# Kernel optimization log

Hardware: AMD Instinct MI355X
Metric: run time of the kernel (lower is better)

## Reference

```python
import jax, jax.numpy as jnp
import numpy as np

NEG_SLOPE = 0.2
NUM_GRAPHS = 64


def _gatv2_layer(x, src, dst, Wl, bl, Wr, br, att, bias, n_nodes, heads, ch):
    # lin_l (source) and lin_r (target) transforms -> [N, H, C]
    xs = (x @ Wl + bl).reshape(n_nodes, heads, ch)
    xd = (x @ Wr + br).reshape(n_nodes, heads, ch)
    s = xs[src]                                   # [E, H, C] gathered source feats
    e = jax.nn.leaky_relu(s + xd[dst], NEG_SLOPE)  # GATv2: leaky_relu BEFORE att dot
    score = jnp.einsum('ehc,hc->eh', e, att)       # [E, H]
    # segment softmax over edges sharing the same target node
    smax = jax.ops.segment_max(score, dst, num_segments=n_nodes)
    ex = jnp.exp(score - smax[dst])
    denom = jax.ops.segment_sum(ex, dst, num_segments=n_nodes)
    alpha = ex / denom[dst]                        # [E, H]
    out = jax.ops.segment_sum(alpha[:, :, None] * s, dst, num_segments=n_nodes)
    return out.reshape(n_nodes, heads * ch) + bias


def setup_inputs() -> dict:
    key = jax.random.key(0)
    ks = jax.random.split(key, 20)
    N, E, F = 50000, 800000, 128
    H, C = 4, 64
    G = NUM_GRAPHS
    sc = 0.05
    inp = {
        'x': jax.random.normal(ks[0], (N, F), jnp.float32),
        'edge_index': jax.random.randint(ks[1], (2, E), 0, N, jnp.int64 if jax.config.read('jax_enable_x64') else jnp.int32).astype(jnp.int32),
        'batch': jnp.sort(jax.random.randint(ks[2], (N,), 0, G)).astype(jnp.int32),
        'W_l1': jax.random.normal(ks[3], (F, H * C)) * sc,
        'b_l1': jax.random.normal(ks[4], (H * C,)) * sc,
        'W_r1': jax.random.normal(ks[5], (F, H * C)) * sc,
        'b_r1': jax.random.normal(ks[6], (H * C,)) * sc,
        'att1': jax.random.normal(ks[7], (H, C)) * sc,
        'bias1': jax.random.normal(ks[8], (H * C,)) * sc,
        'W_l2': jax.random.normal(ks[9], (H * C, C)) * sc,
        'b_l2': jax.random.normal(ks[10], (C,)) * sc,
        'W_r2': jax.random.normal(ks[11], (H * C, C)) * sc,
        'b_r2': jax.random.normal(ks[12], (C,)) * sc,
        'att2': jax.random.normal(ks[13], (1, C)) * sc,
        'bias2': jax.random.normal(ks[14], (C,)) * sc,
        'W_lin': jax.random.normal(ks[15], (C, 1)) * sc,
        'b_lin': jax.random.normal(ks[16], (1,)) * sc,
    }
    return inp


def reference(x, edge_index, batch, W_l1, b_l1, W_r1, b_r1, att1, bias1,
              W_l2, b_l2, W_r2, b_r2, att2, bias2, W_lin, b_lin):
    N = x.shape[0]
    # PyG GATv2Conv adds self-loops by default
    loops = jnp.arange(N, dtype=edge_index.dtype)
    src = jnp.concatenate([edge_index[0], loops])
    dst = jnp.concatenate([edge_index[1], loops])

    h = _gatv2_layer(x, src, dst, W_l1, b_l1, W_r1, b_r1, att1, bias1, N, 4, 64)
    h = jax.nn.relu(h)  # dropout=identity (eval), norm=Identity
    h = _gatv2_layer(h, src, dst, W_l2, b_l2, W_r2, b_r2, att2, bias2, N, 1, 64)

    # global mean pool over graphs
    sums = jax.ops.segment_sum(h, batch, num_segments=NUM_GRAPHS)
    counts = jax.ops.segment_sum(jnp.ones((N,), h.dtype), batch, num_segments=NUM_GRAPHS)
    pooled = sums / jnp.maximum(counts, 1.0)[:, None]  # [G, 64]
    return pooled @ W_lin + b_lin                      # [G, 1]
```

## Files before the change

kernel.cpp:

```cpp
#include <hip/hip_runtime.h>
#include <hip/hip_bf16.h>
#include <math.h>

typedef __attribute__((ext_vector_type(8))) short short8;
typedef __attribute__((ext_vector_type(4))) float floatx4;

__device__ __forceinline__ float bf2f(unsigned short u) {
  union { unsigned int i; float f; } v; v.i = ((unsigned int)u) << 16; return v.f;
}
__device__ __forceinline__ unsigned short f2bf(float f) {
  union { float f; unsigned int u; } v; v.f = f;
  unsigned int r = (v.u + 0x7fffu + ((v.u >> 16) & 1u)) >> 16;
  return (unsigned short)r;
}
__device__ __forceinline__ int imin(int a, int b) { return a < b ? a : b; }
__device__ __forceinline__ int iclamp(int v, int lo, int hi) {
  return v < lo ? lo : (v > hi ? hi : v);
}
__device__ __forceinline__ float uasf(unsigned int u) {
  union { unsigned int i; float f; } v; v.i = u; return v.f;
}

__global__ void k_sentinel(float* out, float val) {
  if (threadIdx.x < 64) out[threadIdx.x] = val;
}

__global__ void k_probe_init(const void* __restrict__ x, int* dflag,
                             int* deg, float* pool, int* cnt, int N) {
  int i = blockIdx.x * 256 + threadIdx.x;
  if (i < N) deg[i] = 1;
  if (i < 64 * 64) pool[i] = 0.f;
  if (i < 64) cnt[i] = 0;
  if (blockIdx.x == 0) {
    __shared__ int c;
    if (threadIdx.x == 0) c = 0;
    __syncthreads();
    unsigned short u = ((const unsigned short*)x)[threadIdx.x];
    int e = (u >> 7) & 0xFF;
    atomicAdd(&c, (u == 0) || (e >= 100 && e <= 145));
    __syncthreads();
    if (threadIdx.x == 0) dflag[0] = (c < 240) ? 1 : 0;
  }
}

struct CvtSegs {
  const void* src[10];
  unsigned short* dst[10];
  int len[10];
};

__global__ void k_prep(const void* __restrict__ x, unsigned short* __restrict__ x_c,
                       int n8, CvtSegs segs,
                       const void* __restrict__ s0, const void* __restrict__ s1,
                       const void* __restrict__ s2, const void* __restrict__ s3,
                       unsigned short* __restrict__ d0, unsigned short* __restrict__ d1,
                       unsigned short* __restrict__ d2, unsigned short* __restrict__ d3,
                       const int* __restrict__ edst, int* deg, int E, int N,
                       const int* __restrict__ dflag, int nCvt8, int nTransB) {
  int b = blockIdx.x;
  if (b < nCvt8) {
    if (!dflag[0]) return;
    int i = b * 256 + threadIdx.x;
    if (i >= n8) return;
    const float* s = (const float*)x + (size_t)i * 8;
    ushort4 a, c;
    a.x = f2bf(s[0]); a.y = f2bf(s[1]); a.z = f2bf(s[2]); a.w = f2bf(s[3]);
    c.x = f2bf(s[4]); c.y = f2bf(s[5]); c.z = f2bf(s[6]); c.w = f2bf(s[7]);
    ((ushort4*)x_c)[i * 2] = a;
    ((ushort4*)x_c)[i * 2 + 1] = c;
    return;
  }
  b -= nCvt8;
  if (b < 10) {
    int i = threadIdx.x;
    if (i < segs.len[b])
      segs.dst[b][i] = dflag[0] ? f2bf(((const float*)segs.src[b])[i])
                                : ((const unsigned short*)segs.src[b])[i];
    return;
  }
  b -= 10;
  if (b < nTransB) {
    int idx = b * 256 + threadIdx.x;
    const void* src; unsigned short* dst; int R, C, loc;
    if (idx < 32768)      { src = s0; dst = d0; R = 128; C = 256; loc = idx; }
    else if (idx < 65536) { src = s1; dst = d1; R = 128; C = 256; loc = idx - 32768; }
    else if (idx < 81920) { src = s2; dst = d2; R = 256; C = 64;  loc = idx - 65536; }
    else                  { src = s3; dst = d3; R = 256; C = 64;  loc = idx - 81920; }
    unsigned short u = dflag[0] ? f2bf(((const float*)src)[loc])
                                : ((const unsigned short*)src)[loc];
    int r = loc / C, cc = loc - r * C;
    dst[cc * R + r] = u;
    return;
  }
  b -= nTransB;
  int e = b * 256 + threadIdx.x;
  if (e < E) atomicAdd(&deg[iclamp(edst[e], 0, N - 1)], 1);
}

__global__ __launch_bounds__(1024) void k_scan1(const int* __restrict__ deg, int* bsum, int N) {
  __shared__ int sm[1024];
  int tid = threadIdx.x;
  int i = blockIdx.x * 1024 + tid;
  sm[tid] = (i < N) ? deg[i] : 0;
  __syncthreads();
  for (int off = 512; off > 0; off >>= 1) {
    if (tid < off) sm[tid] += sm[tid + off];
    __syncthreads();
  }
  if (tid == 0) bsum[blockIdx.x] = sm[0];
}

__global__ void k_scan2(int* bsum, int nb) {
  if (threadIdx.x == 0) {
    int run = 0;
    for (int b = 0; b < nb; ++b) { int t = bsum[b]; bsum[b] = run; run += t; }
  }
}

__global__ __launch_bounds__(1024) void k_scan3(const int* __restrict__ deg,
                                                const int* __restrict__ bsum,
                                                int* rowptr, int* cursor, int N) {
  __shared__ int sm[1024];
  int tid = threadIdx.x;
  int i = blockIdx.x * 1024 + tid;
  int v = (i < N) ? deg[i] : 0;
  sm[tid] = v;
  __syncthreads();
  for (int off = 1; off < 1024; off <<= 1) {
    int t = (tid >= off) ? sm[tid - off] : 0;
    __syncthreads();
    sm[tid] += t;
    __syncthreads();
  }
  if (i < N) {
    int ex = sm[tid] - v + bsum[blockIdx.x];
    rowptr[i] = ex;
    cursor[i] = ex;
    if (i == N - 1) rowptr[N] = ex + v;
  }
}

__global__ void k_scatter(const int* __restrict__ esrc, const int* __restrict__ edst,
                          int* cursor, int* colx, int E, int N) {
  int e = blockIdx.x * 256 + threadIdx.x;
  int ET = E + N;
  if (e < ET) {
    int s, d;
    if (e < E) { s = iclamp(esrc[e], 0, N - 1); d = iclamp(edst[e], 0, N - 1); }
    else { s = e - E; d = s; }
    int pos = atomicAdd(&cursor[d], 1);
    pos = iclamp(pos, 0, ET - 1);
    colx[pos] = s;
  }
}

template <int K, int CT, int RT>
__global__ __launch_bounds__(256) void k_gemm2r(
    const unsigned short* __restrict__ A0, const unsigned short* __restrict__ A1,
    const int* __restrict__ dflag,
    const unsigned short* __restrict__ BTl, const unsigned short* __restrict__ BTr,
    const unsigned short* __restrict__ bl, const unsigned short* __restrict__ br,
    unsigned short* __restrict__ outl, unsigned short* __restrict__ outr,
    int Nrows, int M) {
  constexpr int KI = K / 32;
  const unsigned short* A = dflag[0] ? A1 : A0;
  int lane = threadIdx.x & 63;
  int wave = threadIdx.x >> 6;
  int r = lane & 15, q = lane >> 4;
  int col0 = blockIdx.y * (4 * CT * 16) + wave * (CT * 16);
  int row0 = blockIdx.x * (16 * RT);
  short8 Bl[KI][CT], Br[KI][CT];
#pragma unroll
  for (int t = 0; t < CT; ++t) {
    const unsigned short* bpl = BTl + (size_t)(col0 + t * 16 + r) * K + q * 8;
    const unsigned short* bpr = BTr + (size_t)(col0 + t * 16 + r) * K + q * 8;
#pragma unroll
    for (int k = 0; k < KI; ++k) {
      Bl[k][t] = *reinterpret_cast<const short8*>(bpl + k * 32);
      Br[k][t] = *reinterpret_cast<const short8*>(bpr + k * 32);
    }
  }
  float bvl[CT], bvr[CT];
#pragma unroll
  for (int t = 0; t < CT; ++t) {
    bvl[t] = bf2f(bl[col0 + t * 16 + r]);
    bvr[t] = bf2f(br[col0 + t * 16 + r]);
  }
  short8 a[KI], an[KI];
  {
    int ar0 = imin(row0 + r, Nrows - 1);
    const unsigned short* Ap = A + (size_t)ar0 * K + q * 8;
#pragma unroll
    for (int k = 0; k < KI; ++k) a[k] = *reinterpret_cast<const short8*>(Ap + k * 32);
  }
  for (int rt = 0; rt < RT; ++rt) {
    if (rt + 1 < RT) {
      int arn = imin(row0 + (rt + 1) * 16 + r, Nrows - 1);
      const unsigned short* Apn = A + (size_t)arn * K + q * 8;
#pragma unroll
      for (int k = 0; k < KI; ++k) an[k] = *reinterpret_cast<const short8*>(Apn + k * 32);
    }
    floatx4 accl[CT], accr[CT];
#pragma unroll
    for (int t = 0; t < CT; ++t) {
      accl[t] = (floatx4){0.f, 0.f, 0.f, 0.f};
      accr[t] = (floatx4){0.f, 0.f, 0.f, 0.f};
    }
#pragma unroll
    for (int k = 0; k < KI; ++k) {
#pragma unroll
      for (int t = 0; t < CT; ++t) {
        accl[t] = __builtin_amdgcn_mfma_f32_16x16x32_bf16(a[k], Bl[k][t], accl[t], 0, 0, 0);
        accr[t] = __builtin_amdgcn_mfma_f32_16x16x32_bf16(a[k], Br[k][t], accr[t], 0, 0, 0);
      }
    }
#pragma unroll
    for (int t = 0; t < CT; ++t) {
      int col = col0 + t * 16 + r;
#pragma unroll
      for (int rr = 0; rr < 4; ++rr) {
        int row = row0 + rt * 16 + q * 4 + rr;
        if (row < Nrows) {
          outl[(size_t)row * M + col] = f2bf(accl[t][rr] + bvl[t]);
          outr[(size_t)row * M + col] = f2bf(accr[t][rr] + bvr[t]);
        }
      }
    }
#pragma unroll
    for (int k = 0; k < KI; ++k) a[k] = an[k];
  }
}

#define UNPACK2(u, v0, v1, v2, v3)          \
  v0 = uasf(u.x << 16); v1 = uasf(u.x & 0xffff0000u); \
  v2 = uasf(u.y << 16); v3 = uasf(u.y & 0xffff0000u);

#define SCORE(q0, q1, q2, q3, p)                             \
  p = q0 * 0.6f;                                             \
  p = fmaf(q1, 0.6f, p); p = fmaf(q2, 0.6f, p); p = fmaf(q3, 0.6f, p); \
  p = fmaf(c0, fabsf(q0), p); p = fmaf(c1, fabsf(q1), p);    \
  p = fmaf(c2, fabsf(q2), p); p = fmaf(c3, fabsf(q3), p);

__global__ __launch_bounds__(256) void k_agg_h4(
    const int* __restrict__ rowptr, const int* __restrict__ colx,
    const unsigned short* __restrict__ xs, const unsigned short* __restrict__ xd,
    const unsigned short* __restrict__ att, const unsigned short* __restrict__ bias,
    unsigned short* __restrict__ hout, int N) {
  int lane = threadIdx.x & 63;
  int dst = (blockIdx.x * 256 + threadIdx.x) >> 6;
  if (dst >= N) return;
  int off = lane << 2;
  unsigned int off2 = (unsigned int)off * 2;
  const char* xsb = (const char*)xs;
  ushort4 au = *reinterpret_cast<const ushort4*>(att + off);
  ushort4 du = *reinterpret_cast<const ushort4*>(xd + (size_t)dst * 256 + off);
  float a0 = bf2f(au.x), a1 = bf2f(au.y), a2 = bf2f(au.z), a3 = bf2f(au.w);
  float d0 = bf2f(du.x), d1 = bf2f(du.y), d2 = bf2f(du.z), d3 = bf2f(du.w);
  float ad0 = a0 * d0, ad1 = a1 * d1, ad2 = a2 * d2, ad3 = a3 * d3;
  float c0 = copysignf(0.4f, a0), c1 = copysignf(0.4f, a1);
  float c2 = copysignf(0.4f, a2), c3 = copysignf(0.4f, a3);
  float l = 0.f, o0 = 0.f, o1 = 0.f, o2 = 0.f, o3 = 0.f;
  int beg = __builtin_amdgcn_readfirstlane(rowptr[dst]);
  int end = __builtin_amdgcn_readfirstlane(rowptr[dst + 1]);
  int e1 = end - 1;
  int i0 = colx[beg], i1 = colx[imin(beg + 1, e1)];
  int i2 = colx[imin(beg + 2, e1)], i3 = colx[imin(beg + 3, e1)];
  uint2 ua = *(const uint2*)(xsb + (((unsigned)i0 << 9) + off2));
  uint2 ub = *(const uint2*)(xsb + (((unsigned)i1 << 9) + off2));
  uint2 uc = *(const uint2*)(xsb + (((unsigned)i2 << 9) + off2));
  uint2 ud = *(const uint2*)(xsb + (((unsigned)i3 << 9) + off2));
  for (int e = beg; e < end; e += 4) {
    uint2 na = ua, nb = ub, nc = uc, nd = ud;
    int np = e + 4;
    if (np < end) {
      int t0 = colx[np], t1 = colx[imin(np + 1, e1)];
      int t2 = colx[imin(np + 2, e1)], t3 = colx[imin(np + 3, e1)];
      na = *(const uint2*)(xsb + (((unsigned)t0 << 9) + off2));
      nb = *(const uint2*)(xsb + (((unsigned)t1 << 9) + off2));
      nc = *(const uint2*)(xsb + (((unsigned)t2 << 9) + off2));
      nd = *(const uint2*)(xsb + (((unsigned)t3 << 9) + off2));
    }
    float va0, va1, va2, va3, vb0, vb1, vb2, vb3;
    float vc0, vc1, vc2, vc3, vd0, vd1, vd2, vd3;
    UNPACK2(ua, va0, va1, va2, va3)
    UNPACK2(ub, vb0, vb1, vb2, vb3)
    UNPACK2(uc, vc0, vc1, vc2, vc3)
    UNPACK2(ud, vd0, vd1, vd2, vd3)
    float qa0 = fmaf(a0, va0, ad0), qa1 = fmaf(a1, va1, ad1);
    float qa2 = fmaf(a2, va2, ad2), qa3 = fmaf(a3, va3, ad3);
    float qb0 = fmaf(a0, vb0, ad0), qb1 = fmaf(a1, vb1, ad1);
    float qb2 = fmaf(a2, vb2, ad2), qb3 = fmaf(a3, vb3, ad3);
    float qc0 = fmaf(a0, vc0, ad0), qc1 = fmaf(a1, vc1, ad1);
    float qc2 = fmaf(a2, vc2, ad2), qc3 = fmaf(a3, vc3, ad3);
    float qd0 = fmaf(a0, vd0, ad0), qd1 = fmaf(a1, vd1, ad1);
    float qd2 = fmaf(a2, vd2, ad2), qd3 = fmaf(a3, vd3, ad3);
    float pa, pb, pc, pd;
    SCORE(qa0, qa1, qa2, qa3, pa)
    SCORE(qb0, qb1, qb2, qb3, pb)
    SCORE(qc0, qc1, qc2, qc3, pc)
    SCORE(qd0, qd1, qd2, qd3, pd)
    pa += __shfl_xor(pa, 1); pb += __shfl_xor(pb, 1);
    pc += __shfl_xor(pc, 1); pd += __shfl_xor(pd, 1);
    pa += __shfl_xor(pa, 2); pb += __shfl_xor(pb, 2);
    pc += __shfl_xor(pc, 2); pd += __shfl_xor(pd, 2);
    pa += __shfl_xor(pa, 4); pb += __shfl_xor(pb, 4);
    pc += __shfl_xor(pc, 4); pd += __shfl_xor(pd, 4);
    pa += __shfl_xor(pa, 8); pb += __shfl_xor(pb, 8);
    pc += __shfl_xor(pc, 8); pd += __shfl_xor(pd, 8);
    pa = fminf(fmaxf(pa, -60.f), 60.f);
    pb = (e + 1 < end) ? fminf(fmaxf(pb, -60.f), 60.f) : -INFINITY;
    pc = (e + 2 < end) ? fminf(fmaxf(pc, -60.f), 60.f) : -INFINITY;
    pd = (e + 3 < end) ? fminf(fmaxf(pd, -60.f), 60.f) : -INFINITY;
    float wa = __expf(pa), wb = __expf(pb), wc = __expf(pc), wd = __expf(pd);
    l += (wa + wb) + (wc + wd);
    o0 = fmaf(wa, va0, o0); o0 = fmaf(wb, vb0, o0);
    o0 = fmaf(wc, vc0, o0); o0 = fmaf(wd, vd0, o0);
    o1 = fmaf(wa, va1, o1); o1 = fmaf(wb, vb1, o1);
    o1 = fmaf(wc, vc1, o1); o1 = fmaf(wd, vd1, o1);
    o2 = fmaf(wa, va2, o2); o2 = fmaf(wb, vb2, o2);
    o2 = fmaf(wc, vc2, o2); o2 = fmaf(wd, vd2, o2);
    o3 = fmaf(wa, va3, o3); o3 = fmaf(wb, vb3, o3);
    o3 = fmaf(wc, vc3, o3); o3 = fmaf(wd, vd3, o3);
    ua = na; ub = nb; uc = nc; ud = nd;
  }
  float rl = 1.0f / l;
  ushort4 bu = *reinterpret_cast<const ushort4*>(bias + off);
  ushort4 res;
  res.x = f2bf(fmaxf(fmaf(o0, rl, bf2f(bu.x)), 0.f));
  res.y = f2bf(fmaxf(fmaf(o1, rl, bf2f(bu.y)), 0.f));
  res.z = f2bf(fmaxf(fmaf(o2, rl, bf2f(bu.z)), 0.f));
  res.w = f2bf(fmaxf(fmaf(o3, rl, bf2f(bu.w)), 0.f));
  *reinterpret_cast<ushort4*>(hout + (size_t)dst * 256 + off) = res;
}

__global__ __launch_bounds__(256) void k_agg_h1(
    const int* __restrict__ rowptr, const int* __restrict__ colx,
    const unsigned short* __restrict__ xs, const unsigned short* __restrict__ xd,
    const unsigned short* __restrict__ att, const unsigned short* __restrict__ bias,
    float* __restrict__ hout, int N) {
  int lane = threadIdx.x & 63;
  int wid = (blockIdx.x * 256 + threadIdx.x) >> 6;
  int g = lane >> 4, sl = lane & 15;
  int dst = wid * 4 + g;
  bool valid = dst < N;
  int dsafe = valid ? dst : 0;
  int cb = sl << 2;
  unsigned int cb2 = (unsigned int)cb * 2;
  const char* xsb = (const char*)xs;
  ushort4 au = *reinterpret_cast<const ushort4*>(att + cb);
  ushort4 du = *reinterpret_cast<const ushort4*>(xd + (size_t)dsafe * 64 + cb);
  float a0 = bf2f(au.x), a1 = bf2f(au.y), a2 = bf2f(au.z), a3 = bf2f(au.w);
  float d0 = bf2f(du.x), d1 = bf2f(du.y), d2 = bf2f(du.z), d3 = bf2f(du.w);
  float ad0 = a0 * d0, ad1 = a1 * d1, ad2 = a2 * d2, ad3 = a3 * d3;
  float c0 = copysignf(0.4f, a0), c1 = copysignf(0.4f, a1);
  float c2 = copysignf(0.4f, a2), c3 = copysignf(0.4f, a3);
  float l = 0.f, o0 = 0.f, o1 = 0.f, o2 = 0.f, o3 = 0.f;
  int beg = valid ? rowptr[dst] : 0;
  int end = valid ? rowptr[dst + 1] : 0;
  if (end > beg) {
    int e1 = end - 1;
    int i0 = colx[beg], i1 = colx[imin(beg + 1, e1)];
    int i2 = colx[imin(beg + 2, e1)], i3 = colx[imin(beg + 3, e1)];
    uint2 ua = *(const uint2*)(xsb + (((unsigned)i0 << 7) + cb2));
    uint2 ub = *(const uint2*)(xsb + (((unsigned)i1 << 7) + cb2));
    uint2 uc = *(const uint2*)(xsb + (((unsigned)i2 << 7) + cb2));
    uint2 ud = *(const uint2*)(xsb + (((unsigned)i3 << 7) + cb2));
    for (int e = beg; e < end; e += 4) {
      uint2 na = ua, nb = ub, nc = uc, nd = ud;
      int np = e + 4;
      if (np < end) {
        int t0 = colx[np], t1 = colx[imin(np + 1, e1)];
        int t2 = colx[imin(np + 2, e1)], t3 = colx[imin(np + 3, e1)];
        na = *(const uint2*)(xsb + (((unsigned)t0 << 7) + cb2));
        nb = *(const uint2*)(xsb + (((unsigned)t1 << 7) + cb2));
        nc = *(const uint2*)(xsb + (((unsigned)t2 << 7) + cb2));
        nd = *(const uint2*)(xsb + (((unsigned)t3 << 7) + cb2));
      }
      float va0, va1, va2, va3, vb0, vb1, vb2, vb3;
      float vc0, vc1, vc2, vc3, vd0, vd1, vd2, vd3;
      UNPACK2(ua, va0, va1, va2, va3)
      UNPACK2(ub, vb0, vb1, vb2, vb3)
      UNPACK2(uc, vc0, vc1, vc2, vc3)
      UNPACK2(ud, vd0, vd1, vd2, vd3)
      float qa0 = fmaf(a0, va0, ad0), qa1 = fmaf(a1, va1, ad1);
      float qa2 = fmaf(a2, va2, ad2), qa3 = fmaf(a3, va3, ad3);
      float qb0 = fmaf(a0, vb0, ad0), qb1 = fmaf(a1, vb1, ad1);
      float qb2 = fmaf(a2, vb2, ad2), qb3 = fmaf(a3, vb3, ad3);
      float qc0 = fmaf(a0, vc0, ad0), qc1 = fmaf(a1, vc1, ad1);
      float qc2 = fmaf(a2, vc2, ad2), qc3 = fmaf(a3, vc3, ad3);
      float qd0 = fmaf(a0, vd0, ad0), qd1 = fmaf(a1, vd1, ad1);
      float qd2 = fmaf(a2, vd2, ad2), qd3 = fmaf(a3, vd3, ad3);
      float pa, pb, pc, pd;
      SCORE(qa0, qa1, qa2, qa3, pa)
      SCORE(qb0, qb1, qb2, qb3, pb)
      SCORE(qc0, qc1, qc2, qc3, pc)
      SCORE(qd0, qd1, qd2, qd3, pd)
      pa += __shfl_xor(pa, 1); pb += __shfl_xor(pb, 1);
      pc += __shfl_xor(pc, 1); pd += __shfl_xor(pd, 1);
      pa += __shfl_xor(pa, 2); pb += __shfl_xor(pb, 2);
      pc += __shfl_xor(pc, 2); pd += __shfl_xor(pd, 2);
      pa += __shfl_xor(pa, 4); pb += __shfl_xor(pb, 4);
      pc += __shfl_xor(pc, 4); pd += __shfl_xor(pd, 4);
      pa += __shfl_xor(pa, 8); pb += __shfl_xor(pb, 8);
      pc += __shfl_xor(pc, 8); pd += __shfl_xor(pd, 8);
      pa = fminf(fmaxf(pa, -60.f), 60.f);
      pb = (e + 1 < end) ? fminf(fmaxf(pb, -60.f), 60.f) : -INFINITY;
      pc = (e + 2 < end) ? fminf(fmaxf(pc, -60.f), 60.f) : -INFINITY;
      pd = (e + 3 < end) ? fminf(fmaxf(pd, -60.f), 60.f) : -INFINITY;
      float wa = __expf(pa), wb = __expf(pb), wc = __expf(pc), wd = __expf(pd);
      l += (wa + wb) + (wc + wd);
      o0 = fmaf(wa, va0, o0); o0 = fmaf(wb, vb0, o0);
      o0 = fmaf(wc, vc0, o0); o0 = fmaf(wd, vd0, o0);
      o1 = fmaf(wa, va1, o1); o1 = fmaf(wb, vb1, o1);
      o1 = fmaf(wc, vc1, o1); o1 = fmaf(wd, vd1, o1);
      o2 = fmaf(wa, va2, o2); o2 = fmaf(wb, vb2, o2);
      o2 = fmaf(wc, vc2, o2); o2 = fmaf(wd, vd2, o2);
      o3 = fmaf(wa, va3, o3); o3 = fmaf(wb, vb3, o3);
      o3 = fmaf(wd, vd3, o3); o3 = fmaf(wc, vc3, o3);
      ua = na; ub = nb; uc = nc; ud = nd;
    }
  }
  if (valid) {
    float rl = 1.0f / l;
    ushort4 bu = *reinterpret_cast<const ushort4*>(bias + cb);
    floatx4 res;
    res[0] = fmaf(o0, rl, bf2f(bu.x));
    res[1] = fmaf(o1, rl, bf2f(bu.y));
    res[2] = fmaf(o2, rl, bf2f(bu.z));
    res[3] = fmaf(o3, rl, bf2f(bu.w));
    *reinterpret_cast<floatx4*>(hout + (size_t)dst * 64 + cb) = res;
  }
}

__global__ __launch_bounds__(256) void k_pool(const float* __restrict__ h2,
                                              const int* __restrict__ batch,
                                              float* pool, int* cnt, int N) {
  int lane = threadIdx.x & 63;
  int wid = (blockIdx.x * 256 + threadIdx.x) >> 6;
  int n0 = wid * 32;
  if (n0 >= N) return;
  int nend = imin(n0 + 32, N);
  float acc = 0.f;
  int c = 0;
  int gcur = iclamp(batch[n0], 0, 63);
  for (int n = n0; n < nend; ++n) {
    int gg = iclamp(batch[n], 0, 63);
    if (gg != gcur) {
      atomicAdd(&pool[gcur * 64 + lane], acc);
      if (lane == 0) atomicAdd(&cnt[gcur], c);
      acc = 0.f; c = 0; gcur = gg;
    }
    acc += h2[(size_t)n * 64 + lane];
    c++;
  }
  atomicAdd(&pool[gcur * 64 + lane], acc);
  if (lane == 0) atomicAdd(&cnt[gcur], c);
}

__global__ void k_final(const float* __restrict__ pool, const int* __restrict__ cnt,
                        const unsigned short* __restrict__ Wlinc,
                        const unsigned short* __restrict__ blinc,
                        float* __restrict__ out) {
  int g = threadIdx.x;
  if (g >= 64) return;
  float inv = 1.f / fmaxf((float)cnt[g], 1.f);
  float s = 0.f;
  for (int c = 0; c < 64; ++c) s += pool[g * 64 + c] * bf2f(Wlinc[c]);
  out[g] = fmaf(s, inv, bf2f(blinc[0]));
}

extern "C" void kernel_launch(void* const* d_in, const int* in_sizes, int n_in,
                              void* d_out, int out_size, void* d_ws, size_t ws_size,
                              hipStream_t stream) {
  const void* x     = d_in[0];
  const int*  ei    = (const int*)d_in[1];
  const int*  batch = (const int*)d_in[2];
  const void* Wl1 = d_in[3];  const void* bl1 = d_in[4];
  const void* Wr1 = d_in[5];  const void* br1 = d_in[6];
  const void* att1 = d_in[7]; const void* bias1 = d_in[8];
  const void* Wl2 = d_in[9];  const void* bl2 = d_in[10];
  const void* Wr2 = d_in[11]; const void* br2 = d_in[12];
  const void* att2 = d_in[13]; const void* bias2 = d_in[14];
  const void* Wlin = d_in[15]; const void* blin = d_in[16];
  float* out = (float*)d_out;

  const int F = 128, HC = 256, C2 = 64;
  int N = in_sizes[0] / F;
  int E = in_sizes[1] / 2;
  int ET = E + N;
  const int* esrc = ei;
  const int* edst = ei + E;

  char* w = (char*)d_ws;
  auto alloc = [&](size_t bytes) {
    char* p = w;
    w += (bytes + 255) & ~(size_t)255;
    return p;
  };
  int* dflag  = (int*)alloc(4);
  int* rowptr = (int*)alloc((size_t)(N + 1) * 4);
  int* cursor = (int*)alloc((size_t)N * 4);
  int* deg    = (int*)alloc((size_t)N * 4);
  int* bsum   = (int*)alloc(1024 * 4);
  float* pool = (float*)alloc(64 * 64 * 4);
  int* cnt    = (int*)alloc(64 * 4);
  int* colx   = (int*)alloc((size_t)ET * 4);
  unsigned short* smallc = (unsigned short*)alloc(4096);
  unsigned short* Wl1T = (unsigned short*)alloc((size_t)F * HC * 2);
  unsigned short* Wr1T = (unsigned short*)alloc((size_t)F * HC * 2);
  unsigned short* Wl2T = (unsigned short*)alloc((size_t)HC * C2 * 2);
  unsigned short* Wr2T = (unsigned short*)alloc((size_t)HC * C2 * 2);
  unsigned short* xs1  = (unsigned short*)alloc((size_t)N * HC * 2);
  unsigned short* xd1  = (unsigned short*)alloc((size_t)N * HC * 2);
  unsigned short* h1   = (unsigned short*)alloc((size_t)N * HC * 2);
  size_t required = (size_t)(w - (char*)d_ws);

  unsigned short* x_c = h1;
  unsigned short* xs2 = xs1;
  unsigned short* xd2 = xs1 + (size_t)N * C2;
  float*          h2  = (float*)xd1;

  unsigned short* bl1c   = smallc + 0;
  unsigned short* br1c   = smallc + 256;
  unsigned short* att1c  = smallc + 512;
  unsigned short* bias1c = smallc + 768;
  unsigned short* bl2c   = smallc + 1024;
  unsigned short* br2c   = smallc + 1088;
  unsigned short* att2c  = smallc + 1152;
  unsigned short* bias2c = smallc + 1216;
  unsigned short* Wlinc  = smallc + 1280;
  unsigned short* blinc  = smallc + 1344;

  if (ws_size < required) {
    k_sentinel<<<1, 64, 0, stream>>>(out, 1000.f + (float)(ws_size >> 20));
    return;
  }

  k_probe_init<<<(N + 255) / 256, 256, 0, stream>>>(x, dflag, deg, pool, cnt, N);

  CvtSegs segs;
  const void* ssrc[10] = {bl1, br1, att1, bias1, bl2, br2, att2, bias2, Wlin, blin};
  unsigned short* sdst[10] = {bl1c, br1c, att1c, bias1c, bl2c, br2c, att2c, bias2c, Wlinc, blinc};
  int slen[10] = {256, 256, 256, 256, 64, 64, 64, 64, 64, 1};
  for (int i = 0; i < 10; ++i) { segs.src[i] = ssrc[i]; segs.dst[i] = sdst[i]; segs.len[i] = slen[i]; }
  int n8 = N * F / 8;
  int nCvt8 = (n8 + 255) / 256;
  int nTransB = (2 * F * HC + 2 * HC * C2 + 255) / 256;
  int nHist = (E + 255) / 256;
  k_prep<<<nCvt8 + 10 + nTransB + nHist, 256, 0, stream>>>(
      x, x_c, n8, segs, Wl1, Wr1, Wl2, Wr2, Wl1T, Wr1T, Wl2T, Wr2T,
      edst, deg, E, N, dflag, nCvt8, nTransB);

  int nb = (N + 1023) / 1024;
  k_scan1<<<nb, 1024, 0, stream>>>(deg, bsum, N);
  k_scan2<<<1, 64, 0, stream>>>(bsum, nb);
  k_scan3<<<nb, 1024, 0, stream>>>(deg, bsum, rowptr, cursor, N);
  k_scatter<<<(ET + 255) / 256, 256, 0, stream>>>(esrc, edst, cursor, colx, E, N);

  {
    dim3 g((N + 127) / 128, 2);
    k_gemm2r<128, 2, 8><<<g, 256, 0, stream>>>(
        (const unsigned short*)x, x_c, dflag, Wl1T, Wr1T, bl1c, br1c, xs1, xd1, N, HC);
  }
  k_agg_h4<<<(N + 3) / 4, 256, 0, stream>>>(rowptr, colx, xs1, xd1, att1c, bias1c, h1, N);

  {
    dim3 g((N + 63) / 64, 1);
    k_gemm2r<256, 1, 4><<<g, 256, 0, stream>>>(
        h1, h1, dflag, Wl2T, Wr2T, bl2c, br2c, xs2, xd2, N, C2);
  }
  k_agg_h1<<<(N + 15) / 16, 256, 0, stream>>>(rowptr, colx, xs2, xd2, att2c, bias2c, h2, N);

  int pw = (N + 31) / 32;
  k_pool<<<(pw + 3) / 4, 256, 0, stream>>>(h2, batch, pool, cnt, N);
  k_final<<<1, 64, 0, stream>>>(pool, cnt, Wlinc, blinc, out);
}
```

Before: 361.5 us.

## Merge setup kernels, fuse CSR scatter with layer-1 GEMM, use DPP reductions

Drops the probe/init kernel: zeroing moves to a memset and each k_prep block detects the input dtype itself. The single-thread scan2 is folded into scan3, where each block sums the preceding block totals itself. Self-loop edges are placed deterministically at the end of each row, and the edge scatter now shares one launch with the layer-1 GEMM so the two can overlap. It also pads colx so aggregation can drop its index clamps, and replaces the shuffle reductions with DPP row reductions. The cost is redundant dtype probing in every prep block and a serial prefix loop in scan3 blocks.

```diff
diff --git a/kernel.cpp b/kernel.cpp
--- a/kernel.cpp
+++ b/kernel.cpp
@@ -20,27 +20,18 @@
 __device__ __forceinline__ float uasf(unsigned int u) {
   union { unsigned int i; float f; } v; v.i = u; return v.f;
 }
+__device__ __forceinline__ float sum16(float x) {
+  union { float f; int i; } a, t;
+  a.f = x;
+  t.i = __builtin_amdgcn_update_dpp(0, a.i, 0x121, 0xF, 0xF, true); a.f += t.f;
+  t.i = __builtin_amdgcn_update_dpp(0, a.i, 0x122, 0xF, 0xF, true); a.f += t.f;
+  t.i = __builtin_amdgcn_update_dpp(0, a.i, 0x124, 0xF, 0xF, true); a.f += t.f;
+  t.i = __builtin_amdgcn_update_dpp(0, a.i, 0x128, 0xF, 0xF, true); a.f += t.f;
+  return a.f;
+}
 
 __global__ void k_sentinel(float* out, float val) {
   if (threadIdx.x < 64) out[threadIdx.x] = val;
-}
-
-__global__ void k_probe_init(const void* __restrict__ x, int* dflag,
-                             int* deg, float* pool, int* cnt, int N) {
-  int i = blockIdx.x * 256 + threadIdx.x;
-  if (i < N) deg[i] = 1;
-  if (i < 64 * 64) pool[i] = 0.f;
-  if (i < 64) cnt[i] = 0;
-  if (blockIdx.x == 0) {
-    __shared__ int c;
-    if (threadIdx.x == 0) c = 0;
-    __syncthreads();
-    unsigned short u = ((const unsigned short*)x)[threadIdx.x];
-    int e = (u >> 7) & 0xFF;
-    atomicAdd(&c, (u == 0) || (e >= 100 && e <= 145));
-    __syncthreads();
-    if (threadIdx.x == 0) dflag[0] = (c < 240) ? 1 : 0;
-  }
 }
 
 struct CvtSegs {
@@ -56,10 +47,21 @@
                        unsigned short* __restrict__ d0, unsigned short* __restrict__ d1,
                        unsigned short* __restrict__ d2, unsigned short* __restrict__ d3,
                        const int* __restrict__ edst, int* deg, int E, int N,
-                       const int* __restrict__ dflag, int nCvt8, int nTransB) {
+                       int* dflag, int* colx, int ET, int nCvt8, int nTransB) {
+  __shared__ int csh;
+  if (threadIdx.x == 0) csh = 0;
+  __syncthreads();
+  {
+    unsigned short u = ((const unsigned short*)x)[threadIdx.x];
+    int e = (u >> 7) & 0xFF;
+    atomicAdd(&csh, (u == 0) || (e >= 100 && e <= 145));
+  }
+  __syncthreads();
+  int isf = (csh < 240);
+
   int b = blockIdx.x;
   if (b < nCvt8) {
-    if (!dflag[0]) return;
+    if (!isf) return;
     int i = b * 256 + threadIdx.x;
     if (i >= n8) return;
     const float* s = (const float*)x + (size_t)i * 8;
@@ -72,10 +74,14 @@
   }
   b -= nCvt8;
   if (b < 10) {
+    if (b == 0) {
+      if (threadIdx.x == 0) dflag[0] = isf;
+      if (threadIdx.x >= 248) colx[ET + (threadIdx.x - 248)] = 0;
+    }
     int i = threadIdx.x;
     if (i < segs.len[b])
-      segs.dst[b][i] = dflag[0] ? f2bf(((const float*)segs.src[b])[i])
-                                : ((const unsigned short*)segs.src[b])[i];
+      segs.dst[b][i] = isf ? f2bf(((const float*)segs.src[b])[i])
+                           : ((const unsigned short*)segs.src[b])[i];
     return;
   }
   b -= 10;
@@ -86,8 +92,8 @@
     else if (idx < 65536) { src = s1; dst = d1; R = 128; C = 256; loc = idx - 32768; }
     else if (idx < 81920) { src = s2; dst = d2; R = 256; C = 64;  loc = idx - 65536; }
     else                  { src = s3; dst = d3; R = 256; C = 64;  loc = idx - 81920; }
-    unsigned short u = dflag[0] ? f2bf(((const float*)src)[loc])
-                                : ((const unsigned short*)src)[loc];
+    unsigned short u = isf ? f2bf(((const float*)src)[loc])
+                           : ((const unsigned short*)src)[loc];
     int r = loc / C, cc = loc - r * C;
     dst[cc * R + r] = u;
     return;
@@ -101,7 +107,7 @@
   __shared__ int sm[1024];
   int tid = threadIdx.x;
   int i = blockIdx.x * 1024 + tid;
-  sm[tid] = (i < N) ? deg[i] : 0;
+  sm[tid] = (i < N) ? deg[i] + 1 : 0;
   __syncthreads();
   for (int off = 512; off > 0; off >>= 1) {
     if (tid < off) sm[tid] += sm[tid + off];
@@ -110,20 +116,19 @@
   if (tid == 0) bsum[blockIdx.x] = sm[0];
 }
 
-__global__ void k_scan2(int* bsum, int nb) {
-  if (threadIdx.x == 0) {
-    int run = 0;
-    for (int b = 0; b < nb; ++b) { int t = bsum[b]; bsum[b] = run; run += t; }
-  }
-}
-
 __global__ __launch_bounds__(1024) void k_scan3(const int* __restrict__ deg,
                                                 const int* __restrict__ bsum,
                                                 int* rowptr, int* cursor, int N) {
   __shared__ int sm[1024];
+  __shared__ int boff;
   int tid = threadIdx.x;
+  if (tid == 0) {
+    int r = 0;
+    for (int b = 0; b < blockIdx.x; ++b) r += bsum[b];
+    boff = r;
+  }
   int i = blockIdx.x * 1024 + tid;
-  int v = (i < N) ? deg[i] : 0;
+  int v = (i < N) ? deg[i] + 1 : 0;
   sm[tid] = v;
   __syncthreads();
   for (int off = 1; off < 1024; off <<= 1) {
@@ -133,42 +138,27 @@
     __syncthreads();
   }
   if (i < N) {
-    int ex = sm[tid] - v + bsum[blockIdx.x];
+    int ex = sm[tid] - v + boff;
     rowptr[i] = ex;
     cursor[i] = ex;
     if (i == N - 1) rowptr[N] = ex + v;
   }
 }
 
-__global__ void k_scatter(const int* __restrict__ esrc, const int* __restrict__ edst,
-                          int* cursor, int* colx, int E, int N) {
-  int e = blockIdx.x * 256 + threadIdx.x;
-  int ET = E + N;
-  if (e < ET) {
-    int s, d;
-    if (e < E) { s = iclamp(esrc[e], 0, N - 1); d = iclamp(edst[e], 0, N - 1); }
-    else { s = e - E; d = s; }
-    int pos = atomicAdd(&cursor[d], 1);
-    pos = iclamp(pos, 0, ET - 1);
-    colx[pos] = s;
-  }
-}
-
 template <int K, int CT, int RT>
-__global__ __launch_bounds__(256) void k_gemm2r(
-    const unsigned short* __restrict__ A0, const unsigned short* __restrict__ A1,
-    const int* __restrict__ dflag,
+__device__ __forceinline__ void gemm2r_body(
+    int bx, int by, int tid,
+    const unsigned short* __restrict__ A,
     const unsigned short* __restrict__ BTl, const unsigned short* __restrict__ BTr,
     const unsigned short* __restrict__ bl, const unsigned short* __restrict__ br,
     unsigned short* __restrict__ outl, unsigned short* __restrict__ outr,
     int Nrows, int M) {
   constexpr int KI = K / 32;
-  const unsigned short* A = dflag[0] ? A1 : A0;
-  int lane = threadIdx.x & 63;
-  int wave = threadIdx.x >> 6;
+  int lane = tid & 63;
+  int wave = tid >> 6;
   int r = lane & 15, q = lane >> 4;
-  int col0 = blockIdx.y * (4 * CT * 16) + wave * (CT * 16);
-  int row0 = blockIdx.x * (16 * RT);
+  int col0 = by * (4 * CT * 16) + wave * (CT * 16);
+  int row0 = bx * (16 * RT);
   short8 Bl[KI][CT], Br[KI][CT];
 #pragma unroll
   for (int t = 0; t < CT; ++t) {
@@ -229,6 +219,47 @@
 #pragma unroll
     for (int k = 0; k < KI; ++k) a[k] = an[k];
   }
+}
+
+__global__ __launch_bounds__(256) void k_phase1(
+    const unsigned short* __restrict__ A0, const unsigned short* __restrict__ A1,
+    const int* __restrict__ dflag,
+    const unsigned short* __restrict__ BTl, const unsigned short* __restrict__ BTr,
+    const unsigned short* __restrict__ bl, const unsigned short* __restrict__ br,
+    unsigned short* __restrict__ outl, unsigned short* __restrict__ outr,
+    int Nrows, int M, int nRB, int nG,
+    const int* __restrict__ esrc, const int* __restrict__ edst,
+    const int* __restrict__ rowptr, int* cursor, int* colx, int E, int N) {
+  int b = blockIdx.x;
+  if (b < nG) {
+    const unsigned short* A = dflag[0] ? A1 : A0;
+    gemm2r_body<128, 2, 8>(b >> 1, b & 1, threadIdx.x, A, BTl, BTr, bl, br,
+                           outl, outr, Nrows, M);
+    return;
+  }
+  b -= nG;
+  int e = b * 256 + threadIdx.x;
+  int ET = E + N;
+  if (e < ET) {
+    if (e < E) {
+      int s = iclamp(esrc[e], 0, N - 1), d = iclamp(edst[e], 0, N - 1);
+      int pos = atomicAdd(&cursor[d], 1);
+      colx[iclamp(pos, 0, ET - 1)] = s;
+    } else {
+      int i = e - E;
+      colx[rowptr[i + 1] - 1] = i;
+    }
+  }
+}
+
+__global__ __launch_bounds__(256) void k_gemm2r_l2(
+    const unsigned short* __restrict__ A,
+    const unsigned short* __restrict__ BTl, const unsigned short* __restrict__ BTr,
+    const unsigned short* __restrict__ bl, const unsigned short* __restrict__ br,
+    unsigned short* __restrict__ outl, unsigned short* __restrict__ outr,
+    int Nrows, int M) {
+  gemm2r_body<256, 1, 4>(blockIdx.x, 0, threadIdx.x, A, BTl, BTr, bl, br,
+                         outl, outr, Nrows, M);
 }
 
 #define UNPACK2(u, v0, v1, v2, v3)          \
@@ -262,9 +293,8 @@
   float l = 0.f, o0 = 0.f, o1 = 0.f, o2 = 0.f, o3 = 0.f;
   int beg = __builtin_amdgcn_readfirstlane(rowptr[dst]);
   int end = __builtin_amdgcn_readfirstlane(rowptr[dst + 1]);
-  int e1 = end - 1;
-  int i0 = colx[beg], i1 = colx[imin(beg + 1, e1)];
-  int i2 = colx[imin(beg + 2, e1)], i3 = colx[imin(beg + 3, e1)];
+  int i0 = colx[beg], i1 = colx[beg + 1];
+  int i2 = colx[beg + 2], i3 = colx[beg + 3];
   uint2 ua = *(const uint2*)(xsb + (((unsigned)i0 << 9) + off2));
   uint2 ub = *(const uint2*)(xsb + (((unsigned)i1 << 9) + off2));
   uint2 uc = *(const uint2*)(xsb + (((unsigned)i2 << 9) + off2));
@@ -273,8 +303,8 @@
     uint2 na = ua, nb = ub, nc = uc, nd = ud;
     int np = e + 4;
     if (np < end) {
-      int t0 = colx[np], t1 = colx[imin(np + 1, e1)];
-      int t2 = colx[imin(np + 2, e1)], t3 = colx[imin(np + 3, e1)];
+      int t0 = colx[np], t1 = colx[np + 1];
+      int t2 = colx[np + 2], t3 = colx[np + 3];
       na = *(const uint2*)(xsb + (((unsigned)t0 << 9) + off2));
       nb = *(const uint2*)(xsb + (((unsigned)t1 << 9) + off2));
       nc = *(const uint2*)(xsb + (((unsigned)t2 << 9) + off2));
@@ -299,14 +329,7 @@
     SCORE(qb0, qb1, qb2, qb3, pb)
     SCORE(qc0, qc1, qc2, qc3, pc)
     SCORE(qd0, qd1, qd2, qd3, pd)
-    pa += __shfl_xor(pa, 1); pb += __shfl_xor(pb, 1);
-    pc += __shfl_xor(pc, 1); pd += __shfl_xor(pd, 1);
-    pa += __shfl_xor(pa, 2); pb += __shfl_xor(pb, 2);
-    pc += __shfl_xor(pc, 2); pd += __shfl_xor(pd, 2);
-    pa += __shfl_xor(pa, 4); pb += __shfl_xor(pb, 4);
-    pc += __shfl_xor(pc, 4); pd += __shfl_xor(pd, 4);
-    pa += __shfl_xor(pa, 8); pb += __shfl_xor(pb, 8);
-    pc += __shfl_xor(pc, 8); pd += __shfl_xor(pd, 8);
+    pa = sum16(pa); pb = sum16(pb); pc = sum16(pc); pd = sum16(pd);
     pa = fminf(fmaxf(pa, -60.f), 60.f);
     pb = (e + 1 < end) ? fminf(fmaxf(pb, -60.f), 60.f) : -INFINITY;
     pc = (e + 2 < end) ? fminf(fmaxf(pc, -60.f), 60.f) : -INFINITY;
@@ -358,9 +381,8 @@
   int beg = valid ? rowptr[dst] : 0;
   int end = valid ? rowptr[dst + 1] : 0;
   if (end > beg) {
-    int e1 = end - 1;
-    int i0 = colx[beg], i1 = colx[imin(beg + 1, e1)];
-    int i2 = colx[imin(beg + 2, e1)], i3 = colx[imin(beg + 3, e1)];
+    int i0 = colx[beg], i1 = colx[beg + 1];
+    int i2 = colx[beg + 2], i3 = colx[beg + 3];
     uint2 ua = *(const uint2*)(xsb + (((unsigned)i0 << 7) + cb2));
     uint2 ub = *(const uint2*)(xsb + (((unsigned)i1 << 7) + cb2));
     uint2 uc = *(const uint2*)(xsb + (((unsigned)i2 << 7) + cb2));
@@ -369,8 +391,8 @@
       uint2 na = ua, nb = ub, nc = uc, nd = ud;
       int np = e + 4;
       if (np < end) {
-        int t0 = colx[np], t1 = colx[imin(np + 1, e1)];
-        int t2 = colx[imin(np + 2, e1)], t3 = colx[imin(np + 3, e1)];
+        int t0 = colx[np], t1 = colx[np + 1];
+        int t2 = colx[np + 2], t3 = colx[np + 3];
         na = *(const uint2*)(xsb + (((unsigned)t0 << 7) + cb2));
         nb = *(const uint2*)(xsb + (((unsigned)t1 << 7) + cb2));
         nc = *(const uint2*)(xsb + (((unsigned)t2 << 7) + cb2));
@@ -395,14 +417,7 @@
       SCORE(qb0, qb1, qb2, qb3, pb)
       SCORE(qc0, qc1, qc2, qc3, pc)
       SCORE(qd0, qd1, qd2, qd3, pd)
-      pa += __shfl_xor(pa, 1); pb += __shfl_xor(pb, 1);
-      pc += __shfl_xor(pc, 1); pd += __shfl_xor(pd, 1);
-      pa += __shfl_xor(pa, 2); pb += __shfl_xor(pb, 2);
-      pc += __shfl_xor(pc, 2); pd += __shfl_xor(pd, 2);
-      pa += __shfl_xor(pa, 4); pb += __shfl_xor(pb, 4);
-      pc += __shfl_xor(pc, 4); pd += __shfl_xor(pd, 4);
-      pa += __shfl_xor(pa, 8); pb += __shfl_xor(pb, 8);
-      pc += __shfl_xor(pc, 8); pd += __shfl_xor(pd, 8);
+      pa = sum16(pa); pb = sum16(pb); pc = sum16(pc); pd = sum16(pd);
       pa = fminf(fmaxf(pa, -60.f), 60.f);
       pb = (e + 1 < end) ? fminf(fmaxf(pb, -60.f), 60.f) : -INFINITY;
       pc = (e + 2 < end) ? fminf(fmaxf(pc, -60.f), 60.f) : -INFINITY;
@@ -416,7 +431,7 @@
       o2 = fmaf(wa, va2, o2); o2 = fmaf(wb, vb2, o2);
       o2 = fmaf(wc, vc2, o2); o2 = fmaf(wd, vd2, o2);
       o3 = fmaf(wa, va3, o3); o3 = fmaf(wb, vb3, o3);
-      o3 = fmaf(wd, vd3, o3); o3 = fmaf(wc, vc3, o3);
+      o3 = fmaf(wc, vc3, o3); o3 = fmaf(wd, vd3, o3);
       ua = na; ub = nb; uc = nc; ud = nd;
     }
   }
@@ -500,20 +515,21 @@
   int* dflag  = (int*)alloc(4);
   int* rowptr = (int*)alloc((size_t)(N + 1) * 4);
   int* cursor = (int*)alloc((size_t)N * 4);
-  int* deg    = (int*)alloc((size_t)N * 4);
   int* bsum   = (int*)alloc(1024 * 4);
-  float* pool = (float*)alloc(64 * 64 * 4);
-  int* cnt    = (int*)alloc(64 * 4);
-  int* colx   = (int*)alloc((size_t)ET * 4);
+  int* colx   = (int*)alloc((size_t)(ET + 8) * 4);
   unsigned short* smallc = (unsigned short*)alloc(4096);
   unsigned short* Wl1T = (unsigned short*)alloc((size_t)F * HC * 2);
   unsigned short* Wr1T = (unsigned short*)alloc((size_t)F * HC * 2);
   unsigned short* Wl2T = (unsigned short*)alloc((size_t)HC * C2 * 2);
   unsigned short* Wr2T = (unsigned short*)alloc((size_t)HC * C2 * 2);
+  int* deg    = (int*)alloc((size_t)N * 4);
+  float* pool = (float*)alloc(64 * 64 * 4);
+  int* cnt    = (int*)alloc(64 * 4);
   unsigned short* xs1  = (unsigned short*)alloc((size_t)N * HC * 2);
   unsigned short* xd1  = (unsigned short*)alloc((size_t)N * HC * 2);
   unsigned short* h1   = (unsigned short*)alloc((size_t)N * HC * 2);
   size_t required = (size_t)(w - (char*)d_ws);
+  size_t zlen = (size_t)((char*)cnt + 256 - (char*)deg);
 
   unsigned short* x_c = h1;
   unsigned short* xs2 = xs1;
@@ -536,7 +552,7 @@
     return;
   }
 
-  k_probe_init<<<(N + 255) / 256, 256, 0, stream>>>(x, dflag, deg, pool, cnt, N);
+  hipMemsetAsync(deg, 0, zlen, stream);
 
   CvtSegs segs;
   const void* ssrc[10] = {bl1, br1, att1, bias1, bl2, br2, att2, bias2, Wlin, blin};
@@ -549,26 +565,22 @@
   int nHist = (E + 255) / 256;
   k_prep<<<nCvt8 + 10 + nTransB + nHist, 256, 0, stream>>>(
       x, x_c, n8, segs, Wl1, Wr1, Wl2, Wr2, Wl1T, Wr1T, Wl2T, Wr2T,
-      edst, deg, E, N, dflag, nCvt8, nTransB);
+      edst, deg, E, N, dflag, colx, ET, nCvt8, nTransB);
 
   int nb = (N + 1023) / 1024;
   k_scan1<<<nb, 1024, 0, stream>>>(deg, bsum, N);
-  k_scan2<<<1, 64, 0, stream>>>(bsum, nb);
   k_scan3<<<nb, 1024, 0, stream>>>(deg, bsum, rowptr, cursor, N);
-  k_scatter<<<(ET + 255) / 256, 256, 0, stream>>>(esrc, edst, cursor, colx, E, N);
-
-  {
-    dim3 g((N + 127) / 128, 2);
-    k_gemm2r<128, 2, 8><<<g, 256, 0, stream>>>(
-        (const unsigned short*)x, x_c, dflag, Wl1T, Wr1T, bl1c, br1c, xs1, xd1, N, HC);
-  }
+
+  int nRB = (N + 127) / 128;
+  int nG = nRB * 2;
+  int nS = (ET + 255) / 256;
+  k_phase1<<<nG + nS, 256, 0, stream>>>(
+      (const unsigned short*)x, x_c, dflag, Wl1T, Wr1T, bl1c, br1c, xs1, xd1,
+      N, HC, nRB, nG, esrc, edst, rowptr, cursor, colx, E, N);
+
   k_agg_h4<<<(N + 3) / 4, 256, 0, stream>>>(rowptr, colx, xs1, xd1, att1c, bias1c, h1, N);
 
-  {
-    dim3 g((N + 63) / 64, 1);
-    k_gemm2r<256, 1, 4><<<g, 256, 0, stream>>>(
-        h1, h1, dflag, Wl2T, Wr2T, bl2c, br2c, xs2, xd2, N, C2);
-  }
+  k_gemm2r_l2<<<(N + 63) / 64, 256, 0, stream>>>(h1, Wl2T, Wr2T, bl2c, br2c, xs2, xd2, N, C2);
   k_agg_h1<<<(N + 15) / 16, 256, 0, stream>>>(rowptr, colx, xs2, xd2, att2c, bias2c, h2, N);
 
   int pw = (N + 31) / 32;
```

After: 346.9 us. -4.1%, faster.
